# Optimization experiments

Measured on AMD Instinct MI355X. Metric: run time of the kernel, lower is better.

## Reference

```python
import jax, jax.numpy as jnp
import numpy as np

N = 50000
E = 1600000
IN_C = 165
HID = 256
HEADS = 8
OUT_C = 2
NEG_SLOPE = 0.2


def setup_inputs() -> dict:
    key = jax.random.key(0)
    ks = jax.random.split(key, 10)
    x = jax.random.normal(ks[0], (N, IN_C), dtype=jnp.float32)
    edge_index = jax.random.randint(ks[1], (2, E), 0, N, dtype=jnp.int64)
    c1 = HID // HEADS  # 32 per-head channels in layer 1
    W1 = jax.random.normal(ks[2], (IN_C, HEADS * c1), dtype=jnp.float32) * (1.0 / np.sqrt(IN_C))
    att_src1 = jax.random.normal(ks[3], (HEADS, c1), dtype=jnp.float32) * 0.1
    att_dst1 = jax.random.normal(ks[4], (HEADS, c1), dtype=jnp.float32) * 0.1
    b1 = jnp.zeros((HEADS * c1,), dtype=jnp.float32)
    W2 = jax.random.normal(ks[5], (HID, 1 * OUT_C), dtype=jnp.float32) * (1.0 / np.sqrt(HID))
    att_src2 = jax.random.normal(ks[6], (1, OUT_C), dtype=jnp.float32) * 0.1
    att_dst2 = jax.random.normal(ks[7], (1, OUT_C), dtype=jnp.float32) * 0.1
    b2 = jnp.zeros((OUT_C,), dtype=jnp.float32)
    return {"x": x, "edge_index": edge_index, "W1": W1, "att_src1": att_src1,
            "att_dst1": att_dst1, "b1": b1, "W2": W2, "att_src2": att_src2,
            "att_dst2": att_dst2, "b2": b2}


def _gat_conv(x, src, dst, W, att_src, att_dst, bias, heads, concat):
    """PyG GATConv (eval mode, self-loops already appended to src/dst)."""
    n = x.shape[0]
    c = att_src.shape[1]
    h = (x @ W).reshape(n, heads, c)                      # [N, H, C]
    a_src = jnp.einsum('nhc,hc->nh', h, att_src)          # [N, H]
    a_dst = jnp.einsum('nhc,hc->nh', h, att_dst)
    e = a_src[src] + a_dst[dst]                           # [Et, H]
    e = jax.nn.leaky_relu(e, NEG_SLOPE)
    # segment softmax over incoming edges of each dst node
    e_max = jax.ops.segment_max(e, dst, num_segments=n)   # [N, H]
    e_exp = jnp.exp(e - e_max[dst])
    denom = jax.ops.segment_sum(e_exp, dst, num_segments=n)
    alpha = e_exp / denom[dst]                            # [Et, H]
    msg = alpha[:, :, None] * h[src]                      # [Et, H, C]
    out = jax.ops.segment_sum(msg, dst, num_segments=n)   # [N, H, C]
    if concat:
        out = out.reshape(n, heads * c)
    else:
        out = out.mean(axis=1)
    return out + bias


def reference(x, edge_index, W1, att_src1, att_dst1, b1, W2, att_src2, att_dst2, b2):
    n = x.shape[0]
    loops = jnp.arange(n, dtype=edge_index.dtype)
    src = jnp.concatenate([edge_index[0], loops])  # add_self_loops=True (PyG default)
    dst = jnp.concatenate([edge_index[1], loops])
    h = _gat_conv(x, src, dst, W1, att_src1, att_dst1, b1, HEADS, True)
    h = jax.nn.elu(h)
    out = _gat_conv(h, src, dst, W2, att_src2, att_dst2, b2, 1, False)
    return out
```

## Files before the change

kernel.cpp:

```cpp
#include <hip/hip_runtime.h>
#include <hip/hip_bf16.h>
#include <math.h>

#define N_NODES 50000
#define N_EDGES 1600000
#define ET (N_EDGES + N_NODES)
#define IN_C 165
#define HID 256
#define HEADS 8
#define C1 32
#define OUT_C 2
#define NEG_SLOPE 0.2f
#define TROWS 32
#define XSTR 36
#define GEMM_BLOCKS ((N_NODES + TROWS - 1) / TROWS)
#define SCB 2048
#define SGRP 256
#define NPP ((N_NODES + 7) / 8)
#define CAPL 96
#define NE4 (N_EDGES / 4)
#define CK 8
#define NCH 21

__device__ inline float lrelu(float v) { return v > 0.f ? v : NEG_SLOPE * v; }

__device__ inline unsigned short f32_bf16(float f) {
    unsigned u = __float_as_uint(f);
    return (unsigned short)((u + 0x7FFFu + ((u >> 16) & 1u)) >> 16);
}

__device__ inline float bflo(unsigned u) { return __uint_as_float(u << 16); }
__device__ inline float bfhi(unsigned u) { return __uint_as_float(u & 0xFFFF0000u); }

__device__ __forceinline__ void gemm1_att_block(
        int row0, const float* __restrict__ x, const float* __restrict__ W,
        const float* __restrict__ att_src, const float* __restrict__ att_dst,
        unsigned short* __restrict__ h, float* __restrict__ a_src,
        float* __restrict__ a_dst, float* xs, float* wb) {
    const int tid = threadIdx.x;
    const int nrow = (N_NODES - row0 < TROWS) ? (N_NODES - row0) : TROWS;
    const int lim = nrow * IN_C;
    for (int idx = tid; idx < TROWS * IN_C; idx += 256) {
        int r = idx / IN_C, k = idx - r * IN_C;
        xs[k * XSTR + r] = (idx < lim) ? x[(size_t)row0 * IN_C + idx] : 0.f;
    }
    const int u  = tid & 31;
    const int kr = tid >> 5;
    {
        const float* ws = W + (size_t)kr * HID + u * 8;
        float4 pa = *(const float4*)(ws);
        float4 pb = *(const float4*)(ws + 4);
        *(float4*)(wb + (kr * 64 + u) * 4)      = pa;
        *(float4*)(wb + (kr * 64 + u + 32) * 4) = pb;
    }
    __syncthreads();

    const int tr = tid >> 5;
    const int cq = tid & 31;
    const int c0 = cq * 8;
    float acc[4][8];
    #pragma unroll
    for (int j = 0; j < 4; ++j)
        #pragma unroll
        for (int q = 0; q < 8; ++q) acc[j][q] = 0.f;

    #pragma unroll 2
    for (int c = 0; c < NCH - 1; ++c) {
        int krow = (c + 1) * CK + kr;
        if (krow > IN_C - 1) krow = IN_C - 1;
        const float* ws = W + (size_t)krow * HID + u * 8;
        float4 pa = *(const float4*)(ws);
        float4 pb = *(const float4*)(ws + 4);
        const float* wcur = wb + (c & 1) * (CK * 256);
        const int k0 = c * CK;
        #pragma unroll
        for (int kk = 0; kk < CK; ++kk) {
            float4 xc = *(const float4*)(xs + (k0 + kk) * XSTR + tr * 4);
            float4 a0 = *(const float4*)(wcur + (kk * 64 + cq) * 4);
            float4 a1 = *(const float4*)(wcur + (kk * 64 + cq + 32) * 4);
            #pragma unroll
            for (int j = 0; j < 4; ++j) {
                float xj = (j == 0) ? xc.x : (j == 1) ? xc.y : (j == 2) ? xc.z : xc.w;
                acc[j][0] += xj * a0.x; acc[j][1] += xj * a0.y;
                acc[j][2] += xj * a0.z; acc[j][3] += xj * a0.w;
                acc[j][4] += xj * a1.x; acc[j][5] += xj * a1.y;
                acc[j][6] += xj * a1.z; acc[j][7] += xj * a1.w;
            }
        }
        float* wnxt = wb + ((c + 1) & 1) * (CK * 256);
        *(float4*)(wnxt + (kr * 64 + u) * 4)      = pa;
        *(float4*)(wnxt + (kr * 64 + u + 32) * 4) = pb;
        __syncthreads();
    }
    {
        const float* wcur = wb + ((NCH - 1) & 1) * (CK * 256);
        const int k0 = (NCH - 1) * CK;
        #pragma unroll
        for (int kk = 0; kk < IN_C - (NCH - 1) * CK; ++kk) {
            float4 xc = *(const float4*)(xs + (k0 + kk) * XSTR + tr * 4);
            float4 a0 = *(const float4*)(wcur + (kk * 64 + cq) * 4);
            float4 a1 = *(const float4*)(wcur + (kk * 64 + cq + 32) * 4);
            #pragma unroll
            for (int j = 0; j < 4; ++j) {
                float xj = (j == 0) ? xc.x : (j == 1) ? xc.y : (j == 2) ? xc.z : xc.w;
                acc[j][0] += xj * a0.x; acc[j][1] += xj * a0.y;
                acc[j][2] += xj * a0.z; acc[j][3] += xj * a0.w;
                acc[j][4] += xj * a1.x; acc[j][5] += xj * a1.y;
                acc[j][6] += xj * a1.z; acc[j][7] += xj * a1.w;
            }
        }
    }
    #pragma unroll
    for (int j = 0; j < 4; ++j) {
        int gr = row0 + tr * 4 + j;
        if (gr < N_NODES) {
            unsigned p[4];
            #pragma unroll
            for (int q = 0; q < 4; ++q)
                p[q] = (unsigned)f32_bf16(acc[j][2*q]) |
                       ((unsigned)f32_bf16(acc[j][2*q+1]) << 16);
            *(uint4*)(h + (size_t)gr * HID + c0) = make_uint4(p[0], p[1], p[2], p[3]);
        }
    }
    {
        const int hd = cq >> 2;
        const float* as = att_src + hd * C1 + (cq & 3) * 8;
        const float* ad = att_dst + hd * C1 + (cq & 3) * 8;
        float av[8], dv[8];
        #pragma unroll
        for (int q = 0; q < 2; ++q) {
            float4 a4 = *(const float4*)(as + q * 4);
            float4 d4 = *(const float4*)(ad + q * 4);
            av[q*4+0]=a4.x; av[q*4+1]=a4.y; av[q*4+2]=a4.z; av[q*4+3]=a4.w;
            dv[q*4+0]=d4.x; dv[q*4+1]=d4.y; dv[q*4+2]=d4.z; dv[q*4+3]=d4.w;
        }
        float ps[4], pd[4];
        #pragma unroll
        for (int j = 0; j < 4; ++j) {
            float s = 0.f, d = 0.f;
            #pragma unroll
            for (int q = 0; q < 8; ++q) {
                s += acc[j][q] * av[q];
                d += acc[j][q] * dv[q];
            }
            ps[j] = s; pd[j] = d;
        }
        #pragma unroll
        for (int off = 1; off <= 2; off <<= 1) {
            #pragma unroll
            for (int j = 0; j < 4; ++j) {
                ps[j] += __shfl_xor(ps[j], off);
                pd[j] += __shfl_xor(pd[j], off);
            }
        }
        if ((cq & 3) == 0) {
            #pragma unroll
            for (int j = 0; j < 4; ++j) {
                int gr = row0 + tr * 4 + j;
                if (gr < N_NODES) {
                    a_src[gr * 8 + hd] = ps[j];
                    a_dst[gr * 8 + hd] = pd[j];
                }
            }
        }
    }
}

__global__ __launch_bounds__(256) void fusedAB_kernel(
        const float* __restrict__ x, const float* __restrict__ W,
        const float* __restrict__ att_src, const float* __restrict__ att_dst,
        unsigned short* __restrict__ h, float* __restrict__ a_src,
        float* __restrict__ a_dst,
        const int* __restrict__ src, const int* __restrict__ dst,
        int* __restrict__ deg, unsigned short* __restrict__ csr) {
    __shared__ float xs[IN_C * XSTR];
    __shared__ float wlds[2 * CK * 256];
    if (blockIdx.x < GEMM_BLOCKS) {
        gemm1_att_block(blockIdx.x * TROWS, x, W, att_src, att_dst,
                        h, a_src, a_dst, xs, wlds);
    } else {
        const int sb  = blockIdx.x - GEMM_BLOCKS;
        const int cls = sb & 7;
        const int blk = sb >> 3;
        const int lo = cls * NPP;
        const int hi = (lo + NPP < N_NODES) ? lo + NPP : N_NODES;
        const int t = blk * 256 + threadIdx.x;
        if (t < hi - lo) {
            int d = lo + t;
            int slot = atomicAdd(&deg[d], 1);
            csr[(size_t)d * CAPL + slot] = (unsigned short)d;
        }
        const int4* dst4 = (const int4*)dst;
        for (int uu = t; uu < NE4; uu += SGRP * 256) {
            int4 dv = dst4[uu];
            #pragma unroll
            for (int j = 0; j < 4; ++j) {
                int d = (j == 0) ? dv.x : (j == 1) ? dv.y : (j == 2) ? dv.z : dv.w;
                if (d >= lo && d < hi) {
                    int slot = atomicAdd(&deg[d], 1);
                    csr[(size_t)d * CAPL + slot] = (unsigned short)src[4 * uu + j];
                }
            }
        }
    }
}

__global__ __launch_bounds__(256) void agg1_fused_kernel(
        const int* __restrict__ deg, const unsigned short* __restrict__ csr,
        const float* __restrict__ a_src, const float* __restrict__ a_dst,
        const unsigned short* __restrict__ h1, const float* __restrict__ bias1,
        const float* __restrict__ W2,
        const float* __restrict__ as2, const float* __restrict__ ad2,
        float4* __restrict__ pk, float* __restrict__ a2d) {
    int wid = (blockIdx.x * 256 + threadIdx.x) >> 6;
    int l = threadIdx.x & 63;
    if (wid >= N_NODES) return;
    const int el = l >> 5;
    const int q  = l & 31;
    const int hd = q >> 2;
    const int ch = q * 8;
    const unsigned short* lst = csr + (size_t)wid * CAPL;
    const int n = deg[wid];
    const float ad_p = a_dst[wid * 8 + hd];
    float den = 0.f;
    float acc[8];
    #pragma unroll
    for (int k = 0; k < 8; ++k) acc[k] = 0.f;
    int i = 0;
    for (; i + 16 <= n; i += 16) {
        int s[8];
        #pragma unroll
        for (int j = 0; j < 8; ++j) s[j] = lst[i + 2 * j + el];
        uint4 v[8];
        #pragma unroll
        for (int j = 0; j < 8; ++j)
            v[j] = *(const uint4*)(h1 + (size_t)s[j] * HID + ch);
        float w[8];
        #pragma unroll
        for (int j = 0; j < 8; ++j)
            w[j] = __expf(lrelu(a_src[s[j] * 8 + hd] + ad_p));
        #pragma unroll
        for (int j = 0; j < 8; ++j) {
            den += w[j];
            acc[0] += w[j] * bflo(v[j].x); acc[1] += w[j] * bfhi(v[j].x);
            acc[2] += w[j] * bflo(v[j].y); acc[3] += w[j] * bfhi(v[j].y);
            acc[4] += w[j] * bflo(v[j].z); acc[5] += w[j] * bfhi(v[j].z);
            acc[6] += w[j] * bflo(v[j].w); acc[7] += w[j] * bfhi(v[j].w);
        }
    }
    if (i + 8 <= n) {
        int s[4];
        #pragma unroll
        for (int j = 0; j < 4; ++j) s[j] = lst[i + 2 * j + el];
        uint4 v[4];
        #pragma unroll
        for (int j = 0; j < 4; ++j)
            v[j] = *(const uint4*)(h1 + (size_t)s[j] * HID + ch);
        float w[4];
        #pragma unroll
        for (int j = 0; j < 4; ++j)
            w[j] = __expf(lrelu(a_src[s[j] * 8 + hd] + ad_p));
        #pragma unroll
        for (int j = 0; j < 4; ++j) {
            den += w[j];
            acc[0] += w[j] * bflo(v[j].x); acc[1] += w[j] * bfhi(v[j].x);
            acc[2] += w[j] * bflo(v[j].y); acc[3] += w[j] * bfhi(v[j].y);
            acc[4] += w[j] * bflo(v[j].z); acc[5] += w[j] * bfhi(v[j].z);
            acc[6] += w[j] * bflo(v[j].w); acc[7] += w[j] * bfhi(v[j].w);
        }
        i += 8;
    }
    for (; i < n; i += 2) {
        int e = i + el;
        if (e < n) {
            int s = lst[e];
            uint4 v = *(const uint4*)(h1 + (size_t)s * HID + ch);
            float w = __expf(lrelu(a_src[s * 8 + hd] + ad_p));
            den += w;
            acc[0] += w * bflo(v.x); acc[1] += w * bfhi(v.x);
            acc[2] += w * bflo(v.y); acc[3] += w * bfhi(v.y);
            acc[4] += w * bflo(v.z); acc[5] += w * bfhi(v.z);
            acc[6] += w * bflo(v.w); acc[7] += w * bfhi(v.w);
        }
    }
    den += __shfl_xor(den, 32);
    #pragma unroll
    for (int k = 0; k < 8; ++k) acc[k] += __shfl_xor(acc[k], 32);

    const float inv = 1.f / den;
    float4 bva = *(const float4*)(bias1 + ch);
    float4 bvb = *(const float4*)(bias1 + ch + 4);
    float o[8];
    o[0] = acc[0] * inv + bva.x; o[1] = acc[1] * inv + bva.y;
    o[2] = acc[2] * inv + bva.z; o[3] = acc[3] * inv + bva.w;
    o[4] = acc[4] * inv + bvb.x; o[5] = acc[5] * inv + bvb.y;
    o[6] = acc[6] * inv + bvb.z; o[7] = acc[7] * inv + bvb.w;
    #pragma unroll
    for (int k = 0; k < 8; ++k) o[k] = o[k] > 0.f ? o[k] : expm1f(o[k]);
    const float* wv = W2 + q * 16;
    float4 w0 = *(const float4*)(wv);
    float4 w1 = *(const float4*)(wv + 4);
    float4 w2 = *(const float4*)(wv + 8);
    float4 w3 = *(const float4*)(wv + 12);
    float p0 = o[0]*w0.x + o[1]*w0.z + o[2]*w1.x + o[3]*w1.z
             + o[4]*w2.x + o[5]*w2.z + o[6]*w3.x + o[7]*w3.z;
    float p1 = o[0]*w0.y + o[1]*w0.w + o[2]*w1.y + o[3]*w1.w
             + o[4]*w2.y + o[5]*w2.w + o[6]*w3.y + o[7]*w3.w;
    #pragma unroll
    for (int off = 16; off; off >>= 1) {
        p0 += __shfl_xor(p0, off);
        p1 += __shfl_xor(p1, off);
    }
    if (l == 0) {
        pk[wid] = make_float4(p0, p1, p0 * as2[0] + p1 * as2[1], 0.f);
        a2d[wid] = p0 * ad2[0] + p1 * ad2[1];
    }
}

__global__ __launch_bounds__(256) void agg2_fused_kernel(
        const int* __restrict__ deg, const unsigned short* __restrict__ csr,
        const float4* __restrict__ pk, const float* __restrict__ a2d,
        const float* __restrict__ b2, float* __restrict__ out) {
    int t = blockIdx.x * 256 + threadIdx.x;
    int node = t >> 4;
    int l = t & 15;
    if (node >= N_NODES) return;
    const unsigned short* lst = csr + (size_t)node * CAPL;
    const int n = deg[node];
    const float adv = a2d[node];
    float sm = 0.f, acc0 = 0.f, acc1 = 0.f;
    int i = l;
    for (; i + 16 < n; i += 32) {
        int s0 = lst[i], s1 = lst[i + 16];
        float4 p0 = pk[s0], p1 = pk[s1];
        float w0 = __expf(lrelu(p0.z + adv));
        float w1 = __expf(lrelu(p1.z + adv));
        sm += w0 + w1;
        acc0 += w0 * p0.x + w1 * p1.x;
        acc1 += w0 * p0.y + w1 * p1.y;
    }
    for (; i < n; i += 16) {
        int s = lst[i];
        float4 pv = pk[s];
        float w = __expf(lrelu(pv.z + adv));
        sm += w;
        acc0 += w * pv.x;
        acc1 += w * pv.y;
    }
    #pragma unroll
    for (int off = 8; off; off >>= 1) {
        sm   += __shfl_xor(sm, off);
        acc0 += __shfl_xor(acc0, off);
        acc1 += __shfl_xor(acc1, off);
    }
    if (l == 0) {
        *(float2*)(out + node * 2) =
            make_float2(acc0 / sm + b2[0], acc1 / sm + b2[1]);
    }
}

extern "C" void kernel_launch(void* const* d_in, const int* in_sizes, int n_in,
                              void* d_out, int out_size, void* d_ws, size_t ws_size,
                              hipStream_t stream) {
    (void)in_sizes; (void)n_in; (void)out_size; (void)ws_size;
    const float* x        = (const float*)d_in[0];
    const int*   ei       = (const int*)d_in[1];
    const float* W1       = (const float*)d_in[2];
    const float* att_src1 = (const float*)d_in[3];
    const float* att_dst1 = (const float*)d_in[4];
    const float* b1       = (const float*)d_in[5];
    const float* W2       = (const float*)d_in[6];
    const float* att_src2 = (const float*)d_in[7];
    const float* att_dst2 = (const float*)d_in[8];
    const float* b2       = (const float*)d_in[9];
    float* out = (float*)d_out;

    const int* src = ei;
    const int* dst = ei + N_EDGES;

    char* ws = (char*)d_ws;
    size_t off = 0;
    unsigned short* h1 = (unsigned short*)(ws + off);
    off += (size_t)N_NODES * HID * 2;
    float* a_src1 = (float*)(ws + off); off += (size_t)N_NODES * HEADS * 4;
    float* a_dst1 = (float*)(ws + off); off += (size_t)N_NODES * HEADS * 4;
    float4* pk = (float4*)(ws + off); off += (size_t)N_NODES * 16;
    float* a2d = (float*)(ws + off); off += (size_t)N_NODES * 4;
    int* deg    = (int*)(ws + off); off += (size_t)N_NODES * 4;
    unsigned short* csr = (unsigned short*)(ws + off);
    off += (size_t)N_NODES * CAPL * 2;

    hipMemsetAsync(deg, 0, (size_t)N_NODES * 4, stream);

    const int NW = (N_NODES * 64 + 255) / 256;

    fusedAB_kernel<<<GEMM_BLOCKS + SCB, 256, 0, stream>>>(
        x, W1, att_src1, att_dst1, h1, a_src1, a_dst1, src, dst, deg, csr);

    agg1_fused_kernel<<<NW, 256, 0, stream>>>(
        deg, csr, a_src1, a_dst1, h1, b1, W2, att_src2, att_dst2, pk, a2d);

    agg2_fused_kernel<<<(N_NODES * 16 + 255) / 256, 256, 0, stream>>>(
        deg, csr, pk, a2d, b2, out);
}
```

Before: 339.7 us.

## Double-buffer x tiles in GEMM1 and grow register tile to 8x8

The first-layer GEMM tile grows from 32 to 64 rows, so each thread now holds an 8x8 accumulator instead of 4x8. The full 165-column x tile is no longer staged in shared memory up front; x is streamed in 8-column chunks and double-buffered alongside the W chunks. This cuts LDS usage and raises arithmetic intensity per LDS load. The launch bound asks for 4 blocks per SM, but the larger accumulator raises register pressure and halves the number of GEMM blocks.

Result: slower. 785.3 us (+131.2%).

```diff
diff --git a/kernel.cpp b/kernel.cpp
--- a/kernel.cpp
+++ b/kernel.cpp
@@ -11,8 +11,7 @@
 #define C1 32
 #define OUT_C 2
 #define NEG_SLOPE 0.2f
-#define TROWS 32
-#define XSTR 36
+#define TROWS 64
 #define GEMM_BLOCKS ((N_NODES + TROWS - 1) / TROWS)
 #define SCB 2048
 #define SGRP 256
@@ -36,83 +35,99 @@
         int row0, const float* __restrict__ x, const float* __restrict__ W,
         const float* __restrict__ att_src, const float* __restrict__ att_dst,
         unsigned short* __restrict__ h, float* __restrict__ a_src,
-        float* __restrict__ a_dst, float* xs, float* wb) {
+        float* __restrict__ a_dst, float* wb, float* xb) {
     const int tid = threadIdx.x;
-    const int nrow = (N_NODES - row0 < TROWS) ? (N_NODES - row0) : TROWS;
-    const int lim = nrow * IN_C;
-    for (int idx = tid; idx < TROWS * IN_C; idx += 256) {
-        int r = idx / IN_C, k = idx - r * IN_C;
-        xs[k * XSTR + r] = (idx < lim) ? x[(size_t)row0 * IN_C + idx] : 0.f;
-    }
     const int u  = tid & 31;
     const int kr = tid >> 5;
+    const int xrow = tid >> 2;
+    const int xk   = (tid & 3) * 2;
+    const int grow = row0 + xrow;
+    const bool rok = grow < N_NODES;
     {
-        const float* ws = W + (size_t)kr * HID + u * 8;
-        float4 pa = *(const float4*)(ws);
-        float4 pb = *(const float4*)(ws + 4);
+        const float* wsrc = W + (size_t)kr * HID + u * 8;
+        float4 pa = *(const float4*)(wsrc);
+        float4 pb = *(const float4*)(wsrc + 4);
         *(float4*)(wb + (kr * 64 + u) * 4)      = pa;
         *(float4*)(wb + (kr * 64 + u + 32) * 4) = pb;
+        float2 xv = rok ? *(const float2*)(x + (size_t)grow * IN_C + xk)
+                        : make_float2(0.f, 0.f);
+        xb[xk * 64 + xrow]       = xv.x;
+        xb[(xk + 1) * 64 + xrow] = xv.y;
     }
     __syncthreads();
 
     const int tr = tid >> 5;
     const int cq = tid & 31;
     const int c0 = cq * 8;
-    float acc[4][8];
-    #pragma unroll
-    for (int j = 0; j < 4; ++j)
+    float acc[8][8];
+    #pragma unroll
+    for (int j = 0; j < 8; ++j)
         #pragma unroll
         for (int q = 0; q < 8; ++q) acc[j][q] = 0.f;
 
-    #pragma unroll 2
     for (int c = 0; c < NCH - 1; ++c) {
         int krow = (c + 1) * CK + kr;
         if (krow > IN_C - 1) krow = IN_C - 1;
-        const float* ws = W + (size_t)krow * HID + u * 8;
-        float4 pa = *(const float4*)(ws);
-        float4 pb = *(const float4*)(ws + 4);
+        const float* wsrc = W + (size_t)krow * HID + u * 8;
+        float4 pa = *(const float4*)(wsrc);
+        float4 pb = *(const float4*)(wsrc + 4);
+        float xf0 = 0.f, xf1 = 0.f;
+        {
+            int kn = (c + 1) * CK + xk;
+            if (rok) {
+                if (kn + 1 < IN_C) {
+                    float2 t = *(const float2*)(x + (size_t)grow * IN_C + kn);
+                    xf0 = t.x; xf1 = t.y;
+                } else if (kn < IN_C) {
+                    xf0 = x[(size_t)grow * IN_C + kn];
+                }
+            }
+        }
         const float* wcur = wb + (c & 1) * (CK * 256);
-        const int k0 = c * CK;
+        const float* xcur = xb + (c & 1) * (CK * 64);
         #pragma unroll
         for (int kk = 0; kk < CK; ++kk) {
-            float4 xc = *(const float4*)(xs + (k0 + kk) * XSTR + tr * 4);
-            float4 a0 = *(const float4*)(wcur + (kk * 64 + cq) * 4);
-            float4 a1 = *(const float4*)(wcur + (kk * 64 + cq + 32) * 4);
-            #pragma unroll
-            for (int j = 0; j < 4; ++j) {
-                float xj = (j == 0) ? xc.x : (j == 1) ? xc.y : (j == 2) ? xc.z : xc.w;
-                acc[j][0] += xj * a0.x; acc[j][1] += xj * a0.y;
-                acc[j][2] += xj * a0.z; acc[j][3] += xj * a0.w;
-                acc[j][4] += xj * a1.x; acc[j][5] += xj * a1.y;
-                acc[j][6] += xj * a1.z; acc[j][7] += xj * a1.w;
-            }
-        }
-        float* wnxt = wb + ((c + 1) & 1) * (CK * 256);
-        *(float4*)(wnxt + (kr * 64 + u) * 4)      = pa;
-        *(float4*)(wnxt + (kr * 64 + u + 32) * 4) = pb;
+            float4 xa  = *(const float4*)(xcur + kk * 64 + tr * 8);
+            float4 xb4 = *(const float4*)(xcur + kk * 64 + tr * 8 + 4);
+            float4 wa  = *(const float4*)(wcur + (kk * 64 + cq) * 4);
+            float4 wb4 = *(const float4*)(wcur + (kk * 64 + cq + 32) * 4);
+            float xr[8] = {xa.x, xa.y, xa.z, xa.w, xb4.x, xb4.y, xb4.z, xb4.w};
+            float wr[8] = {wa.x, wa.y, wa.z, wa.w, wb4.x, wb4.y, wb4.z, wb4.w};
+            #pragma unroll
+            for (int j = 0; j < 8; ++j)
+                #pragma unroll
+                for (int q = 0; q < 8; ++q)
+                    acc[j][q] += xr[j] * wr[q];
+        }
+        float* wn = wb + ((c + 1) & 1) * (CK * 256);
+        float* xn = xb + ((c + 1) & 1) * (CK * 64);
+        *(float4*)(wn + (kr * 64 + u) * 4)      = pa;
+        *(float4*)(wn + (kr * 64 + u + 32) * 4) = pb;
+        xn[xk * 64 + xrow]       = xf0;
+        xn[(xk + 1) * 64 + xrow] = xf1;
         __syncthreads();
     }
     {
         const float* wcur = wb + ((NCH - 1) & 1) * (CK * 256);
-        const int k0 = (NCH - 1) * CK;
+        const float* xcur = xb + ((NCH - 1) & 1) * (CK * 64);
         #pragma unroll
         for (int kk = 0; kk < IN_C - (NCH - 1) * CK; ++kk) {
-            float4 xc = *(const float4*)(xs + (k0 + kk) * XSTR + tr * 4);
-            float4 a0 = *(const float4*)(wcur + (kk * 64 + cq) * 4);
-            float4 a1 = *(const float4*)(wcur + (kk * 64 + cq + 32) * 4);
-            #pragma unroll
-            for (int j = 0; j < 4; ++j) {
-                float xj = (j == 0) ? xc.x : (j == 1) ? xc.y : (j == 2) ? xc.z : xc.w;
-                acc[j][0] += xj * a0.x; acc[j][1] += xj * a0.y;
-                acc[j][2] += xj * a0.z; acc[j][3] += xj * a0.w;
-                acc[j][4] += xj * a1.x; acc[j][5] += xj * a1.y;
-                acc[j][6] += xj * a1.z; acc[j][7] += xj * a1.w;
-            }
-        }
-    }
-    #pragma unroll
-    for (int j = 0; j < 4; ++j) {
-        int gr = row0 + tr * 4 + j;
+            float4 xa  = *(const float4*)(xcur + kk * 64 + tr * 8);
+            float4 xb4 = *(const float4*)(xcur + kk * 64 + tr * 8 + 4);
+            float4 wa  = *(const float4*)(wcur + (kk * 64 + cq) * 4);
+            float4 wb4 = *(const float4*)(wcur + (kk * 64 + cq + 32) * 4);
+            float xr[8] = {xa.x, xa.y, xa.z, xa.w, xb4.x, xb4.y, xb4.z, xb4.w};
+            float wr[8] = {wa.x, wa.y, wa.z, wa.w, wb4.x, wb4.y, wb4.z, wb4.w};
+            #pragma unroll
+            for (int j = 0; j < 8; ++j)
+                #pragma unroll
+                for (int q = 0; q < 8; ++q)
+                    acc[j][q] += xr[j] * wr[q];
+        }
+    }
+    #pragma unroll
+    for (int j = 0; j < 8; ++j) {
+        int gr = row0 + tr * 8 + j;
         if (gr < N_NODES) {
             unsigned p[4];
             #pragma unroll
@@ -134,9 +149,9 @@
             av[q*4+0]=a4.x; av[q*4+1]=a4.y; av[q*4+2]=a4.z; av[q*4+3]=a4.w;
             dv[q*4+0]=d4.x; dv[q*4+1]=d4.y; dv[q*4+2]=d4.z; dv[q*4+3]=d4.w;
         }
-        float ps[4], pd[4];
-        #pragma unroll
-        for (int j = 0; j < 4; ++j) {
+        float ps[8], pd[8];
+        #pragma unroll
+        for (int j = 0; j < 8; ++j) {
             float s = 0.f, d = 0.f;
             #pragma unroll
             for (int q = 0; q < 8; ++q) {
@@ -148,15 +163,15 @@
         #pragma unroll
         for (int off = 1; off <= 2; off <<= 1) {
             #pragma unroll
-            for (int j = 0; j < 4; ++j) {
+            for (int j = 0; j < 8; ++j) {
                 ps[j] += __shfl_xor(ps[j], off);
                 pd[j] += __shfl_xor(pd[j], off);
             }
         }
         if ((cq & 3) == 0) {
             #pragma unroll
-            for (int j = 0; j < 4; ++j) {
-                int gr = row0 + tr * 4 + j;
+            for (int j = 0; j < 8; ++j) {
+                int gr = row0 + tr * 8 + j;
                 if (gr < N_NODES) {
                     a_src[gr * 8 + hd] = ps[j];
                     a_dst[gr * 8 + hd] = pd[j];
@@ -166,18 +181,18 @@
     }
 }
 
-__global__ __launch_bounds__(256) void fusedAB_kernel(
+__global__ __launch_bounds__(256, 4) void fusedAB_kernel(
         const float* __restrict__ x, const float* __restrict__ W,
         const float* __restrict__ att_src, const float* __restrict__ att_dst,
         unsigned short* __restrict__ h, float* __restrict__ a_src,
         float* __restrict__ a_dst,
         const int* __restrict__ src, const int* __restrict__ dst,
         int* __restrict__ deg, unsigned short* __restrict__ csr) {
-    __shared__ float xs[IN_C * XSTR];
     __shared__ float wlds[2 * CK * 256];
+    __shared__ float xlds[2 * CK * 64];
     if (blockIdx.x < GEMM_BLOCKS) {
         gemm1_att_block(blockIdx.x * TROWS, x, W, att_src, att_dst,
-                        h, a_src, a_dst, xs, wlds);
+                        h, a_src, a_dst, wlds, xlds);
     } else {
         const int sb  = blockIdx.x - GEMM_BLOCKS;
         const int cls = sb & 7;
```

## Split fused GEMM/scatter kernel into separate scatter and GEMM launches

Applied to the files above, without the earlier changes.

Splits the combined kernel, which ran GEMM blocks and CSR-scatter blocks side by side, into two kernels launched one after the other on the same stream: scatter first, then GEMM. The scatter blocks no longer have to reserve the large shared-memory footprint the GEMM path needs, so more of them can be resident and the atomic-heavy scatter may run with higher occupancy. In exchange, the overlap between the compute-bound GEMM and the memory/atomic-bound scatter is lost, and there is an extra launch.

Measured after the change: 373.3 us. +9.9%, slower.

```diff
diff --git a/kernel.cpp b/kernel.cpp
--- a/kernel.cpp
+++ b/kernel.cpp
@@ -32,11 +32,14 @@
 __device__ inline float bflo(unsigned u) { return __uint_as_float(u << 16); }
 __device__ inline float bfhi(unsigned u) { return __uint_as_float(u & 0xFFFF0000u); }
 
-__device__ __forceinline__ void gemm1_att_block(
-        int row0, const float* __restrict__ x, const float* __restrict__ W,
+__global__ __launch_bounds__(256) void gemm1_kernel(
+        const float* __restrict__ x, const float* __restrict__ W,
         const float* __restrict__ att_src, const float* __restrict__ att_dst,
         unsigned short* __restrict__ h, float* __restrict__ a_src,
-        float* __restrict__ a_dst, float* xs, float* wb) {
+        float* __restrict__ a_dst) {
+    __shared__ float xs[IN_C * XSTR];
+    __shared__ float wb[2 * CK * 256];
+    const int row0 = blockIdx.x * TROWS;
     const int tid = threadIdx.x;
     const int nrow = (N_NODES - row0 < TROWS) ? (N_NODES - row0) : TROWS;
     const int lim = nrow * IN_C;
@@ -47,9 +50,9 @@
     const int u  = tid & 31;
     const int kr = tid >> 5;
     {
-        const float* ws = W + (size_t)kr * HID + u * 8;
-        float4 pa = *(const float4*)(ws);
-        float4 pb = *(const float4*)(ws + 4);
+        const float* wsrc = W + (size_t)kr * HID + u * 8;
+        float4 pa = *(const float4*)(wsrc);
+        float4 pb = *(const float4*)(wsrc + 4);
         *(float4*)(wb + (kr * 64 + u) * 4)      = pa;
         *(float4*)(wb + (kr * 64 + u + 32) * 4) = pb;
     }
@@ -68,9 +71,9 @@
     for (int c = 0; c < NCH - 1; ++c) {
         int krow = (c + 1) * CK + kr;
         if (krow > IN_C - 1) krow = IN_C - 1;
-        const float* ws = W + (size_t)krow * HID + u * 8;
-        float4 pa = *(const float4*)(ws);
-        float4 pb = *(const float4*)(ws + 4);
+        const float* wsrc = W + (size_t)krow * HID + u * 8;
+        float4 pa = *(const float4*)(wsrc);
+        float4 pb = *(const float4*)(wsrc + 4);
         const float* wcur = wb + (c & 1) * (CK * 256);
         const int k0 = c * CK;
         #pragma unroll
@@ -87,9 +90,9 @@
                 acc[j][6] += xj * a1.z; acc[j][7] += xj * a1.w;
             }
         }
-        float* wnxt = wb + ((c + 1) & 1) * (CK * 256);
-        *(float4*)(wnxt + (kr * 64 + u) * 4)      = pa;
-        *(float4*)(wnxt + (kr * 64 + u + 32) * 4) = pb;
+        float* wn = wb + ((c + 1) & 1) * (CK * 256);
+        *(float4*)(wn + (kr * 64 + u) * 4)      = pa;
+        *(float4*)(wn + (kr * 64 + u + 32) * 4) = pb;
         __syncthreads();
     }
     {
@@ -166,40 +169,29 @@
     }
 }
 
-__global__ __launch_bounds__(256) void fusedAB_kernel(
-        const float* __restrict__ x, const float* __restrict__ W,
-        const float* __restrict__ att_src, const float* __restrict__ att_dst,
-        unsigned short* __restrict__ h, float* __restrict__ a_src,
-        float* __restrict__ a_dst,
+__global__ __launch_bounds__(256) void scatter_kernel(
         const int* __restrict__ src, const int* __restrict__ dst,
         int* __restrict__ deg, unsigned short* __restrict__ csr) {
-    __shared__ float xs[IN_C * XSTR];
-    __shared__ float wlds[2 * CK * 256];
-    if (blockIdx.x < GEMM_BLOCKS) {
-        gemm1_att_block(blockIdx.x * TROWS, x, W, att_src, att_dst,
-                        h, a_src, a_dst, xs, wlds);
-    } else {
-        const int sb  = blockIdx.x - GEMM_BLOCKS;
-        const int cls = sb & 7;
-        const int blk = sb >> 3;
-        const int lo = cls * NPP;
-        const int hi = (lo + NPP < N_NODES) ? lo + NPP : N_NODES;
-        const int t = blk * 256 + threadIdx.x;
-        if (t < hi - lo) {
-            int d = lo + t;
-            int slot = atomicAdd(&deg[d], 1);
-            csr[(size_t)d * CAPL + slot] = (unsigned short)d;
-        }
-        const int4* dst4 = (const int4*)dst;
-        for (int uu = t; uu < NE4; uu += SGRP * 256) {
-            int4 dv = dst4[uu];
-            #pragma unroll
-            for (int j = 0; j < 4; ++j) {
-                int d = (j == 0) ? dv.x : (j == 1) ? dv.y : (j == 2) ? dv.z : dv.w;
-                if (d >= lo && d < hi) {
-                    int slot = atomicAdd(&deg[d], 1);
-                    csr[(size_t)d * CAPL + slot] = (unsigned short)src[4 * uu + j];
-                }
+    const int sb  = blockIdx.x;
+    const int cls = sb & 7;
+    const int blk = sb >> 3;
+    const int lo = cls * NPP;
+    const int hi = (lo + NPP < N_NODES) ? lo + NPP : N_NODES;
+    const int t = blk * 256 + threadIdx.x;
+    if (t < hi - lo) {
+        int d = lo + t;
+        int slot = atomicAdd(&deg[d], 1);
+        csr[(size_t)d * CAPL + slot] = (unsigned short)d;
+    }
+    const int4* dst4 = (const int4*)dst;
+    for (int uu = t; uu < NE4; uu += SGRP * 256) {
+        int4 dv = dst4[uu];
+        #pragma unroll
+        for (int j = 0; j < 4; ++j) {
+            int d = (j == 0) ? dv.x : (j == 1) ? dv.y : (j == 2) ? dv.z : dv.w;
+            if (d >= lo && d < hi) {
+                int slot = atomicAdd(&deg[d], 1);
+                csr[(size_t)d * CAPL + slot] = (unsigned short)src[4 * uu + j];
             }
         }
     }
@@ -394,8 +386,10 @@
 
     const int NW = (N_NODES * 64 + 255) / 256;
 
-    fusedAB_kernel<<<GEMM_BLOCKS + SCB, 256, 0, stream>>>(
-        x, W1, att_src1, att_dst1, h1, a_src1, a_dst1, src, dst, deg, csr);
+    scatter_kernel<<<SCB, 256, 0, stream>>>(src, dst, deg, csr);
+
+    gemm1_kernel<<<GEMM_BLOCKS, 256, 0, stream>>>(
+        x, W1, att_src1, att_dst1, h1, a_src1, a_dst1);
 
     agg1_fused_kernel<<<NW, 256, 0, stream>>>(
         deg, csr, a_src1, a_dst1, h1, b1, W2, att_src2, att_dst2, pk, a2d);
```
